# Optimization experiments

Hardware: AMD Instinct MI355X
Metric: run time of the kernel (lower is better)

Reference implementation:

```python
import jax, jax.numpy as jnp
import numpy as np

B, T, D, H = 4, 2048, 1024, 16
HD = D // H

def setup_inputs() -> dict:
    key = jax.random.key(0)
    ks = jax.random.split(key, 7)
    s = 1.0 / np.sqrt(D)
    return {
        "x": jax.random.normal(ks[0], (B, T, D), dtype=jnp.float32),
        "w_qkv": jax.random.uniform(ks[1], (D, 3 * D), jnp.float32, -s, s),
        "b_qkv": jax.random.uniform(ks[2], (3 * D,), jnp.float32, -s, s),
        "w_proj": jax.random.uniform(ks[3], (D, D), jnp.float32, -s, s),
        "b_proj": jax.random.uniform(ks[4], (D,), jnp.float32, -s, s),
        "ln_gamma": jnp.ones((D,), jnp.float32),
        "ln_beta": jnp.zeros((D,), jnp.float32),
    }

def reference(x, w_qkv, b_qkv, w_proj, b_proj, ln_gamma, ln_beta):
    eps = 1e-5
    scale = HD ** -0.5
    residual = x
    # Pre-norm LayerNorm over last dim
    mu = jnp.mean(x, axis=-1, keepdims=True)
    var = jnp.mean(jnp.square(x - mu), axis=-1, keepdims=True)
    xn = (x - mu) * jax.lax.rsqrt(var + eps) * ln_gamma + ln_beta
    # QKV projection: (B,T,3D) -> (3,B,H,T,HD)
    qkv = xn @ w_qkv + b_qkv
    qkv = qkv.reshape(B, T, 3, H, HD).transpose(2, 0, 3, 1, 4)
    q, k, v = qkv[0], qkv[1], qkv[2]
    # Scaled dot-product attention (full T x T scores, as in source)
    attn = jnp.einsum('bhqd,bhkd->bhqk', q, k) * scale
    attn = jax.nn.softmax(attn, axis=-1)
    out = jnp.einsum('bhqk,bhkd->bhqd', attn, v)
    out = out.transpose(0, 2, 1, 3).reshape(B, T, D)
    out = out @ w_proj + b_proj
    return residual + out
```

## Files before the change

kernel.cpp:

```cpp
#include <hip/hip_runtime.h>
#include <cstdint>
#include <cstddef>

#define B_ 4
#define T_ 2048
#define D_ 1024
#define H_ 16

typedef __attribute__((ext_vector_type(8))) short short8;
typedef __attribute__((ext_vector_type(4))) float f32x4;
typedef __attribute__((ext_vector_type(8))) unsigned short u16x8;

__device__ __forceinline__ unsigned short f2b16(float f) {
  union { float f; unsigned int u; } un; un.f = f;
  unsigned int r = un.u + 0x7fffu + ((un.u >> 16) & 1u);
  return (unsigned short)(r >> 16);
}
__device__ __forceinline__ void async_cp16(const void* g, void* l) {
  __builtin_amdgcn_global_load_lds((const __attribute__((address_space(1))) void*)g,
                                   (__attribute__((address_space(3))) void*)l,
                                   16, 0, 0);
}
__device__ __forceinline__ f32x4 mfma16(short8 a, short8 b, f32x4 c) {
  return __builtin_amdgcn_mfma_f32_16x16x32_bf16(a, b, c, 0, 0, 0);
}

__global__ __launch_bounds__(256) void ln_kernel(const float* __restrict__ x,
                                                 const float* __restrict__ gamma,
                                                 const float* __restrict__ beta,
                                                 unsigned short* __restrict__ xn) {
  const int row = blockIdx.x;
  const int t = threadIdx.x;
  const float4 v = ((const float4*)(x + (size_t)row * D_))[t];
  float s  = v.x + v.y + v.z + v.w;
  float s2 = v.x*v.x + v.y*v.y + v.z*v.z + v.w*v.w;
  #pragma unroll
  for (int off = 32; off > 0; off >>= 1) {
    s  += __shfl_down(s, off);
    s2 += __shfl_down(s2, off);
  }
  __shared__ float sh[8];
  const int wv = t >> 6, lane = t & 63;
  if (lane == 0) { sh[wv] = s; sh[4 + wv] = s2; }
  __syncthreads();
  if (t == 0) {
    float ts  = sh[0] + sh[1] + sh[2] + sh[3];
    float ts2 = sh[4] + sh[5] + sh[6] + sh[7];
    float mu  = ts * (1.0f / D_);
    float var = ts2 * (1.0f / D_) - mu * mu;
    sh[0] = mu;
    sh[1] = rsqrtf(var + 1e-5f);
  }
  __syncthreads();
  const float mu = sh[0], rs = sh[1];
  const float4 g  = ((const float4*)gamma)[t];
  const float4 bb = ((const float4*)beta)[t];
  ushort4 o;
  o.x = f2b16((v.x - mu) * rs * g.x + bb.x);
  o.y = f2b16((v.y - mu) * rs * g.y + bb.y);
  o.z = f2b16((v.z - mu) * rs * g.z + bb.z);
  o.w = f2b16((v.w - mu) * rs * g.w + bb.w);
  ((ushort4*)(xn + (size_t)row * D_))[t] = o;
}

__global__ __launch_bounds__(256) void transpose_cast(const float* __restrict__ w,
                                                      unsigned short* __restrict__ wT,
                                                      int K, int N) {
  __shared__ float tile[32][33];
  const int n0 = blockIdx.x * 32;
  const int k0 = blockIdx.y * 32;
  const int tx = threadIdx.x, ty = threadIdx.y;
  #pragma unroll
  for (int i = 0; i < 32; i += 8)
    tile[ty + i][tx] = w[(size_t)(k0 + ty + i) * N + n0 + tx];
  __syncthreads();
  #pragma unroll
  for (int i = 0; i < 32; i += 8)
    wT[(size_t)(n0 + ty + i) * K + k0 + tx] = f2b16(tile[tx][ty + i]);
}

__global__ __launch_bounds__(256) void transpose_v(const unsigned short* __restrict__ vB,
                                                   unsigned short* __restrict__ vtB) {
  __shared__ unsigned short tile[64 * 66];
  const int tid = threadIdx.x;
  const int bh = blockIdx.x;
  const int t0 = blockIdx.y * 64;
  const int lr = tid >> 2, lc = (tid & 3) * 16;
  const unsigned short* src = vB + ((size_t)bh * T_ + t0) * 64;
  *(u16x8*)&tile[lr * 66 + lc]     = *(const u16x8*)(src + (size_t)lr * 64 + lc);
  *(u16x8*)&tile[lr * 66 + lc + 8] = *(const u16x8*)(src + (size_t)lr * 64 + lc + 8);
  __syncthreads();
  const int dv = tid >> 2, cb = (tid & 3) * 16;
  unsigned short outv[16];
  #pragma unroll
  for (int j = 0; j < 16; ++j) {
    const int c = cb + j;
    const int t = (c & 32) | ((c & 4) << 2) | ((c & 16) >> 1) | ((c & 8) >> 1) | (c & 3);
    outv[j] = tile[t * 66 + dv];
  }
  unsigned short* dst = vtB + ((size_t)bh * 64 + dv) * T_ + t0 + cb;
  *(u16x8*)dst       = *(const u16x8*)&outv[0];
  *(u16x8*)(dst + 8) = *(const u16x8*)&outv[8];
}

template <int MODE, int NN>
__global__ __launch_bounds__(512, 2) void gemm8p(const unsigned short* __restrict__ A,
                                                 const unsigned short* __restrict__ Bt,
                                                 const float* __restrict__ bias,
                                                 const float* __restrict__ resid,
                                                 unsigned short* __restrict__ qB,
                                                 unsigned short* __restrict__ kB,
                                                 unsigned short* __restrict__ vB,
                                                 float* __restrict__ outF) {
  constexpr int K = 1024;
  constexpr int NT = 16;
  __shared__ __align__(16) unsigned short As[16384];
  __shared__ __align__(16) unsigned short Bs[32768];

  const int tid  = threadIdx.x;
  const int lane = tid & 63;
  const int wv   = tid >> 6;
  const int l15  = lane & 15, quad = lane >> 4;
  const int wr   = wv >> 1;
  const int wc   = wv & 1;

  constexpr int CPX = (64 * (NN / 256)) / 8;
  const int w = (blockIdx.x & 7) * CPX + (blockIdx.x >> 3);
  const int tileM = (w & 63) * 128;
  const int tileN = (w >> 6) * 256;

  const int sr  = tid >> 3;
  const int scs = ((tid & 7) ^ (sr & 7)) * 8;
  const unsigned short* gA = A  + (size_t)(tileM + sr) * K + scs;
  const unsigned short* gB = Bt + (size_t)(tileN + sr) * K + scs;

  auto stA = [&](int h, int ko, int wb) {
    async_cp16(gA + (size_t)(h * 64) * K + ko, &As[wb * 8192 + h * 4096 + tid * 8]);
  };
  auto stB = [&](int h, int ko, int wb) {
    const unsigned short* g = gB + (size_t)(h * 128) * K + ko;
    unsigned short* l = &Bs[wb * 16384 + h * 8192 + tid * 8];
    async_cp16(g, l);
    async_cp16(g + (size_t)64 * K, l + 4096);
  };

  const int rA  = wr * 16 + l15;
  const int rB  = wc * 64 + l15;
  const int ck0 = ((0 + quad) ^ (l15 & 7)) * 8;
  const int ck1 = ((4 + quad) ^ (l15 & 7)) * 8;

  f32x4 acc[2][2][4] = {};

  stA(0, 0, 0); stB(0, 0, 0); stB(1, 0, 0); stA(1, 0, 0);
  asm volatile("s_waitcnt vmcnt(3)" ::: "memory");
  asm volatile("s_barrier" ::: "memory");

  #pragma unroll 2
  for (int kt = 0; kt < NT; ++kt) {
    const int buf = kt & 1;
    const unsigned short* Ab = &As[buf * 8192];
    const unsigned short* Bb = &Bs[buf * 16384];
    const int wb = buf ^ 1;
    const bool st = (kt + 1) < NT;
    const int ko = (kt + 1) * 64;

    short8 a[2], b0[4][2], b1[4][2];

    a[0] = *(const short8*)&Ab[rA * 64 + ck0];
    a[1] = *(const short8*)&Ab[rA * 64 + ck1];
    #pragma unroll
    for (int fn = 0; fn < 4; ++fn) {
      b0[fn][0] = *(const short8*)&Bb[(rB + fn * 16) * 64 + ck0];
      b0[fn][1] = *(const short8*)&Bb[(rB + fn * 16) * 64 + ck1];
    }
    if (st) stA(0, ko, wb);
    asm volatile("s_waitcnt lgkmcnt(0)" ::: "memory");
    __builtin_amdgcn_sched_barrier(0);
    __builtin_amdgcn_s_setprio(1);
    #pragma unroll
    for (int fn = 0; fn < 4; ++fn) {
      acc[0][0][fn] = mfma16(a[0], b0[fn][0], acc[0][0][fn]);
      acc[0][0][fn] = mfma16(a[1], b0[fn][1], acc[0][0][fn]);
    }
    __builtin_amdgcn_s_setprio(0);
    if (st) asm volatile("s_waitcnt vmcnt(2)" ::: "memory");
    else    asm volatile("s_waitcnt vmcnt(1)" ::: "memory");
    asm volatile("s_barrier" ::: "memory");

    #pragma unroll
    for (int fn = 0; fn < 4; ++fn) {
      b1[fn][0] = *(const short8*)&Bb[8192 + (rB + fn * 16) * 64 + ck0];
      b1[fn][1] = *(const short8*)&Bb[8192 + (rB + fn * 16) * 64 + ck1];
    }
    if (st) stB(0, ko, wb);
    asm volatile("s_waitcnt lgkmcnt(0)" ::: "memory");
    __builtin_amdgcn_sched_barrier(0);
    __builtin_amdgcn_s_setprio(1);
    #pragma unroll
    for (int fn = 0; fn < 4; ++fn) {
      acc[0][1][fn] = mfma16(a[0], b1[fn][0], acc[0][1][fn]);
      acc[0][1][fn] = mfma16(a[1], b1[fn][1], acc[0][1][fn]);
    }
    __builtin_amdgcn_s_setprio(0);
    if (st) asm volatile("s_waitcnt vmcnt(3)" ::: "memory");
    else    asm volatile("s_waitcnt vmcnt(0)" ::: "memory");
    asm volatile("s_barrier" ::: "memory");

    a[0] = *(const short8*)&Ab[4096 + rA * 64 + ck0];
    a[1] = *(const short8*)&Ab[4096 + rA * 64 + ck1];
    if (st) stB(1, ko, wb);
    asm volatile("s_waitcnt lgkmcnt(0)" ::: "memory");
    __builtin_amdgcn_sched_barrier(0);
    __builtin_amdgcn_s_setprio(1);
    #pragma unroll
    for (int fn = 0; fn < 4; ++fn) {
      acc[1][0][fn] = mfma16(a[0], b0[fn][0], acc[1][0][fn]);
      acc[1][0][fn] = mfma16(a[1], b0[fn][1], acc[1][0][fn]);
    }
    __builtin_amdgcn_s_setprio(0);
    asm volatile("s_barrier" ::: "memory");

    if (st) stA(1, ko, wb);
    __builtin_amdgcn_s_setprio(1);
    #pragma unroll
    for (int fn = 0; fn < 4; ++fn) {
      acc[1][1][fn] = mfma16(a[0], b1[fn][0], acc[1][1][fn]);
      acc[1][1][fn] = mfma16(a[1], b1[fn][1], acc[1][1][fn]);
    }
    __builtin_amdgcn_s_setprio(0);
    if (st) asm volatile("s_waitcnt vmcnt(3)" ::: "memory");
    asm volatile("s_barrier" ::: "memory");
  }

  if constexpr (MODE == 0) {
    unsigned short* E = &As[wv * 1152];
    #pragma unroll
    for (int qm = 0; qm < 2; ++qm) {
      #pragma unroll
      for (int qn = 0; qn < 2; ++qn) {
        const int colBase = tileN + qn * 128 + wc * 64;
        const int rowBase = tileM + qm * 64 + wr * 16;
        #pragma unroll
        for (int fn = 0; fn < 4; ++fn) {
          const int col = colBase + fn * 16 + l15;
          const float bv = bias[col];
          const float sc = (col < 1024) ? 0.180336880f : 1.0f;
          #pragma unroll
          for (int r = 0; r < 4; ++r)
            E[(quad * 4 + r) * 72 + fn * 16 + l15] =
                f2b16((acc[qm][qn][fn][r] + bv) * sc);
        }
        const int secq = colBase >> 10;
        const int hh   = (colBase & 1023) >> 6;
        unsigned short* outSec = (secq == 0) ? qB : (secq == 1) ? kB : vB;
        #pragma unroll
        for (int it = 0; it < 2; ++it) {
          const int lrow = it * 8 + (lane >> 3);
          const int row = rowBase + lrow;
          const int b_ = row >> 11, t = row & 2047;
          const u16x8 val = *(const u16x8*)&E[lrow * 72 + (lane & 7) * 8];
          *(u16x8*)(outSec + ((size_t)(b_ * 16 + hh) * T_ + t) * 64 + (lane & 7) * 8) = val;
        }
      }
    }
  } else {
    #pragma unroll
    for (int qm = 0; qm < 2; ++qm) {
      #pragma unroll
      for (int qn = 0; qn < 2; ++qn) {
        #pragma unroll
        for (int fn = 0; fn < 4; ++fn) {
          const int col = tileN + qn * 128 + wc * 64 + fn * 16 + l15;
          const float bv = bias[col];
          #pragma unroll
          for (int r = 0; r < 4; ++r) {
            const int row = tileM + qm * 64 + wr * 16 + quad * 4 + r;
            const size_t idx = (size_t)row * NN + col;
            outF[idx] = acc[qm][qn][fn][r] + bv + resid[idx];
          }
        }
      }
    }
  }
}

__global__ __launch_bounds__(256, 4) void attn_mfma(const unsigned short* __restrict__ qB,
                                                    const unsigned short* __restrict__ kB,
                                                    const unsigned short* __restrict__ vtB,
                                                    unsigned short* __restrict__ aout) {
  __shared__ unsigned short Ks[2][64 * 64];
  __shared__ unsigned short Vs[2][64 * 64];

  const int tid = threadIdx.x;
  const int bid = blockIdx.x;
  const int bh = bid & 63;
  const int qb = bid >> 6;
  const int b = bh >> 4, h = bh & 15;
  const int wv = tid >> 6, lane = tid & 63;
  const int l15 = lane & 15, quad = lane >> 4;

  const unsigned short* qP = qB  + (size_t)bh * T_ * 64;
  const unsigned short* kP = kB  + (size_t)bh * T_ * 64;
  const unsigned short* vP = vtB + (size_t)bh * 64 * T_;
  const int q0 = qb * 128 + wv * 32;

  short8 qf[2][2];
  #pragma unroll
  for (int mi = 0; mi < 2; ++mi)
    #pragma unroll
    for (int ks = 0; ks < 2; ++ks)
      qf[mi][ks] = *(const short8*)(qP + ((size_t)(q0 + mi * 16 + l15)) * 64 + ks * 32 + quad * 8);

  const short8 onesf = {0x3F80, 0x3F80, 0x3F80, 0x3F80, 0x3F80, 0x3F80, 0x3F80, 0x3F80};
  f32x4 accO[2][5] = {};

  const int lrow  = lane >> 3;
  const int lchnk = (lane & 7) ^ (lrow & 7);
  const size_t kOff0 = (size_t)((wv * 2 + 0) * 8 + lrow) * 64 + lchnk * 8;
  const size_t kOff1 = (size_t)((wv * 2 + 1) * 8 + lrow) * 64 + lchnk * 8;
  const size_t vOff0 = (size_t)((wv * 2 + 0) * 8 + lrow) * T_ + lchnk * 8;
  const size_t vOff1 = (size_t)((wv * 2 + 1) * 8 + lrow) * T_ + lchnk * 8;
  const int lOff0 = (wv * 2 + 0) * 512 + lane * 8;
  const int lOff1 = (wv * 2 + 1) * 512 + lane * 8;

  async_cp16(kP + kOff0, &Ks[0][lOff0]);
  async_cp16(kP + kOff1, &Ks[0][lOff1]);
  async_cp16(vP + vOff0, &Vs[0][lOff0]);
  async_cp16(vP + vOff1, &Vs[0][lOff1]);
  __syncthreads();

  for (int kt = 0; kt < 32; ++kt) {
    const int buf = kt & 1;
    if (kt + 1 < 32) {
      const unsigned short* kg = kP + (size_t)(kt + 1) * 64 * 64;
      const unsigned short* vg = vP + (kt + 1) * 64;
      async_cp16(kg + kOff0, &Ks[buf ^ 1][lOff0]);
      async_cp16(kg + kOff1, &Ks[buf ^ 1][lOff1]);
      async_cp16(vg + vOff0, &Vs[buf ^ 1][lOff0]);
      async_cp16(vg + vOff1, &Vs[buf ^ 1][lOff1]);
    }
    const unsigned short* K_ = Ks[buf];
    const unsigned short* V_ = Vs[buf];

    f32x4 accT[4][2] = {};
    #pragma unroll
    for (int ks = 0; ks < 2; ++ks) {
      #pragma unroll
      for (int cc = 0; cc < 4; ++cc) {
        const short8 kb = *(const short8*)&K_[(cc * 16 + l15) * 64 +
                                              (((ks << 2) | quad) ^ (l15 & 7)) * 8];
        accT[cc][0] = mfma16(kb, qf[0][ks], accT[cc][0]);
        accT[cc][1] = mfma16(kb, qf[1][ks], accT[cc][1]);
      }
    }

    short8 pa[2][2];
    #pragma unroll
    for (int mi = 0; mi < 2; ++mi) {
      #pragma unroll
      for (int ks = 0; ks < 2; ++ks) {
        union { unsigned short u[8]; short8 s; } pk;
        #pragma unroll
        for (int r = 0; r < 4; ++r) {
          union { float f; unsigned int u; } e0, e1;
          e0.f = __builtin_amdgcn_exp2f(accT[2 * ks + 0][mi][r]);
          e1.f = __builtin_amdgcn_exp2f(accT[2 * ks + 1][mi][r]);
          pk.u[r]     = (unsigned short)(e0.u >> 16);
          pk.u[4 + r] = (unsigned short)(e1.u >> 16);
        }
        pa[mi][ks] = pk.s;
      }
    }

    #pragma unroll
    for (int ks = 0; ks < 2; ++ks) {
      short8 vb[4];
      #pragma unroll
      for (int nj = 0; nj < 4; ++nj)
        vb[nj] = *(const short8*)&V_[(nj * 16 + l15) * 64 +
                                     (((ks << 2) | quad) ^ (l15 & 7)) * 8];
      #pragma unroll
      for (int mi = 0; mi < 2; ++mi) {
        #pragma unroll
        for (int nj = 0; nj < 4; ++nj)
          accO[mi][nj] = mfma16(pa[mi][ks], vb[nj], accO[mi][nj]);
        accO[mi][4] = mfma16(pa[mi][ks], onesf, accO[mi][4]);
      }
    }

    __syncthreads();
  }

  #pragma unroll
  for (int mi = 0; mi < 2; ++mi) {
    #pragma unroll
    for (int r = 0; r < 4; ++r) {
      const float inv = 1.0f / accO[mi][4][r];
      const int row = q0 + mi * 16 + quad * 4 + r;
      unsigned short* op = aout + (size_t)(b * T_ + row) * D_ + h * 64 + l15;
      #pragma unroll
      for (int nj = 0; nj < 4; ++nj)
        op[nj * 16] = f2b16(accO[mi][nj][r] * inv);
    }
  }
}

extern "C" void kernel_launch(void* const* d_in, const int* in_sizes, int n_in,
                              void* d_out, int out_size, void* d_ws, size_t ws_size,
                              hipStream_t stream) {
  const float* x      = (const float*)d_in[0];
  const float* w_qkv  = (const float*)d_in[1];
  const float* b_qkv  = (const float*)d_in[2];
  const float* w_proj = (const float*)d_in[3];
  const float* b_proj = (const float*)d_in[4];
  const float* ln_g   = (const float*)d_in[5];
  const float* ln_b   = (const float*)d_in[6];
  float* out = (float*)d_out;

  char* ws = (char*)d_ws;
  unsigned short* xn   = (unsigned short*)(ws);
  unsigned short* wTq  = (unsigned short*)(ws + (size_t)(16 << 20));
  unsigned short* wTp  = (unsigned short*)(ws + (size_t)(22 << 20));
  unsigned short* qBuf = (unsigned short*)(ws + (size_t)(24 << 20));
  unsigned short* kBuf = (unsigned short*)(ws + (size_t)(40 << 20));
  unsigned short* vBuf = (unsigned short*)(ws + (size_t)(56 << 20));
  unsigned short* vtB  = (unsigned short*)(ws + (size_t)(72 << 20));
  unsigned short* aout = xn;

  ln_kernel<<<8192, 256, 0, stream>>>(x, ln_g, ln_b, xn);
  transpose_cast<<<dim3(96, 32), dim3(32, 8), 0, stream>>>(w_qkv, wTq, 1024, 3072);
  transpose_cast<<<dim3(32, 32), dim3(32, 8), 0, stream>>>(w_proj, wTp, 1024, 1024);
  gemm8p<0, 3072><<<768, 512, 0, stream>>>(xn, wTq, b_qkv, nullptr,
                                           qBuf, kBuf, vBuf, nullptr);
  transpose_v<<<dim3(64, 32), 256, 0, stream>>>(vBuf, vtB);
  attn_mfma<<<1024, 256, 0, stream>>>(qBuf, kBuf, vtB, aout);
  gemm8p<1, 1024><<<256, 512, 0, stream>>>(aout, wTp, b_proj, x,
                                           nullptr, nullptr, nullptr, out);
}
```

Before: 270.2 us.

## Fuse prep kernels, rewrite GEMM with single-buffer tiles, fuse V transpose into epilogue

Merges LayerNorm and both weight transpose-casts into one prep launch. Replaces the hand-pipelined double-buffered GEMM with a simpler single-buffer GEMM: 256x256 tiles for QKV and 128x128 for the output projection, with more blocks per CU. The QKV epilogue now writes V directly in transposed layout through shared memory, so the separate transpose_v kernel is gone. Priority hints are added around the MFMA sections of the attention kernel. The trade-off is that global-to-LDS loads no longer overlap with compute in the GEMM, which may expose memory latency.

```diff
diff --git a/kernel.cpp b/kernel.cpp
--- a/kernel.cpp
+++ b/kernel.cpp
@@ -25,260 +25,242 @@
   return __builtin_amdgcn_mfma_f32_16x16x32_bf16(a, b, c, 0, 0, 0);
 }
 
-__global__ __launch_bounds__(256) void ln_kernel(const float* __restrict__ x,
-                                                 const float* __restrict__ gamma,
-                                                 const float* __restrict__ beta,
-                                                 unsigned short* __restrict__ xn) {
-  const int row = blockIdx.x;
+__global__ __launch_bounds__(256) void prep_kernel(const float* __restrict__ x,
+                                                   const float* __restrict__ gamma,
+                                                   const float* __restrict__ beta,
+                                                   unsigned short* __restrict__ xn,
+                                                   const float* __restrict__ wq,
+                                                   unsigned short* __restrict__ wTq,
+                                                   const float* __restrict__ wp,
+                                                   unsigned short* __restrict__ wTp) {
+  __shared__ float sh[8];
+  __shared__ float tile[32][33];
+  const int bid = blockIdx.x;
   const int t = threadIdx.x;
-  const float4 v = ((const float4*)(x + (size_t)row * D_))[t];
-  float s  = v.x + v.y + v.z + v.w;
-  float s2 = v.x*v.x + v.y*v.y + v.z*v.z + v.w*v.w;
-  #pragma unroll
-  for (int off = 32; off > 0; off >>= 1) {
-    s  += __shfl_down(s, off);
-    s2 += __shfl_down(s2, off);
+
+  if (bid < 8192) {
+    const int row = bid;
+    const float4 v = ((const float4*)(x + (size_t)row * D_))[t];
+    float s  = v.x + v.y + v.z + v.w;
+    float s2 = v.x*v.x + v.y*v.y + v.z*v.z + v.w*v.w;
+    #pragma unroll
+    for (int off = 32; off > 0; off >>= 1) {
+      s  += __shfl_down(s, off);
+      s2 += __shfl_down(s2, off);
+    }
+    const int wv = t >> 6, lane = t & 63;
+    if (lane == 0) { sh[wv] = s; sh[4 + wv] = s2; }
+    __syncthreads();
+    if (t == 0) {
+      float ts  = sh[0] + sh[1] + sh[2] + sh[3];
+      float ts2 = sh[4] + sh[5] + sh[6] + sh[7];
+      float mu  = ts * (1.0f / D_);
+      float var = ts2 * (1.0f / D_) - mu * mu;
+      sh[0] = mu;
+      sh[1] = rsqrtf(var + 1e-5f);
+    }
+    __syncthreads();
+    const float mu = sh[0], rs = sh[1];
+    const float4 g  = ((const float4*)gamma)[t];
+    const float4 bb = ((const float4*)beta)[t];
+    ushort4 o;
+    o.x = f2b16((v.x - mu) * rs * g.x + bb.x);
+    o.y = f2b16((v.y - mu) * rs * g.y + bb.y);
+    o.z = f2b16((v.z - mu) * rs * g.z + bb.z);
+    o.w = f2b16((v.w - mu) * rs * g.w + bb.w);
+    ((ushort4*)(xn + (size_t)row * D_))[t] = o;
+  } else {
+    const float* w; unsigned short* wT; int K, N, bx, by;
+    if (bid < 8192 + 3072) {
+      const int idx = bid - 8192;
+      w = wq; wT = wTq; K = 1024; N = 3072; bx = idx % 96; by = idx / 96;
+    } else {
+      const int idx = bid - 11264;
+      w = wp; wT = wTp; K = 1024; N = 1024; bx = idx % 32; by = idx / 32;
+    }
+    const int n0 = bx * 32, k0 = by * 32;
+    const int tx = t & 31, ty = t >> 5;
+    #pragma unroll
+    for (int i = 0; i < 32; i += 8)
+      tile[ty + i][tx] = w[(size_t)(k0 + ty + i) * N + n0 + tx];
+    __syncthreads();
+    #pragma unroll
+    for (int i = 0; i < 32; i += 8)
+      wT[(size_t)(n0 + ty + i) * K + k0 + tx] = f2b16(tile[tx][ty + i]);
   }
-  __shared__ float sh[8];
-  const int wv = t >> 6, lane = t & 63;
-  if (lane == 0) { sh[wv] = s; sh[4 + wv] = s2; }
-  __syncthreads();
-  if (t == 0) {
-    float ts  = sh[0] + sh[1] + sh[2] + sh[3];
-    float ts2 = sh[4] + sh[5] + sh[6] + sh[7];
-    float mu  = ts * (1.0f / D_);
-    float var = ts2 * (1.0f / D_) - mu * mu;
-    sh[0] = mu;
-    sh[1] = rsqrtf(var + 1e-5f);
-  }
-  __syncthreads();
-  const float mu = sh[0], rs = sh[1];
-  const float4 g  = ((const float4*)gamma)[t];
-  const float4 bb = ((const float4*)beta)[t];
-  ushort4 o;
-  o.x = f2b16((v.x - mu) * rs * g.x + bb.x);
-  o.y = f2b16((v.y - mu) * rs * g.y + bb.y);
-  o.z = f2b16((v.z - mu) * rs * g.z + bb.z);
-  o.w = f2b16((v.w - mu) * rs * g.w + bb.w);
-  ((ushort4*)(xn + (size_t)row * D_))[t] = o;
-}
-
-__global__ __launch_bounds__(256) void transpose_cast(const float* __restrict__ w,
-                                                      unsigned short* __restrict__ wT,
-                                                      int K, int N) {
-  __shared__ float tile[32][33];
-  const int n0 = blockIdx.x * 32;
-  const int k0 = blockIdx.y * 32;
-  const int tx = threadIdx.x, ty = threadIdx.y;
-  #pragma unroll
-  for (int i = 0; i < 32; i += 8)
-    tile[ty + i][tx] = w[(size_t)(k0 + ty + i) * N + n0 + tx];
-  __syncthreads();
-  #pragma unroll
-  for (int i = 0; i < 32; i += 8)
-    wT[(size_t)(n0 + ty + i) * K + k0 + tx] = f2b16(tile[tx][ty + i]);
-}
-
-__global__ __launch_bounds__(256) void transpose_v(const unsigned short* __restrict__ vB,
-                                                   unsigned short* __restrict__ vtB) {
-  __shared__ unsigned short tile[64 * 66];
-  const int tid = threadIdx.x;
-  const int bh = blockIdx.x;
-  const int t0 = blockIdx.y * 64;
-  const int lr = tid >> 2, lc = (tid & 3) * 16;
-  const unsigned short* src = vB + ((size_t)bh * T_ + t0) * 64;
-  *(u16x8*)&tile[lr * 66 + lc]     = *(const u16x8*)(src + (size_t)lr * 64 + lc);
-  *(u16x8*)&tile[lr * 66 + lc + 8] = *(const u16x8*)(src + (size_t)lr * 64 + lc + 8);
-  __syncthreads();
-  const int dv = tid >> 2, cb = (tid & 3) * 16;
-  unsigned short outv[16];
-  #pragma unroll
-  for (int j = 0; j < 16; ++j) {
-    const int c = cb + j;
-    const int t = (c & 32) | ((c & 4) << 2) | ((c & 16) >> 1) | ((c & 8) >> 1) | (c & 3);
-    outv[j] = tile[t * 66 + dv];
-  }
-  unsigned short* dst = vtB + ((size_t)bh * 64 + dv) * T_ + t0 + cb;
-  *(u16x8*)dst       = *(const u16x8*)&outv[0];
-  *(u16x8*)(dst + 8) = *(const u16x8*)&outv[8];
 }
 
 template <int MODE, int NN>
-__global__ __launch_bounds__(512, 2) void gemm8p(const unsigned short* __restrict__ A,
-                                                 const unsigned short* __restrict__ Bt,
-                                                 const float* __restrict__ bias,
-                                                 const float* __restrict__ resid,
-                                                 unsigned short* __restrict__ qB,
-                                                 unsigned short* __restrict__ kB,
-                                                 unsigned short* __restrict__ vB,
-                                                 float* __restrict__ outF) {
-  constexpr int K = 1024;
+__global__ __launch_bounds__(512, 4) void gemm_sb(const unsigned short* __restrict__ A,
+                                                  const unsigned short* __restrict__ Bt,
+                                                  const float* __restrict__ bias,
+                                                  const float* __restrict__ resid,
+                                                  unsigned short* __restrict__ qB,
+                                                  unsigned short* __restrict__ kB,
+                                                  unsigned short* __restrict__ vtB,
+                                                  float* __restrict__ outF) {
+  constexpr int K  = 1024;
   constexpr int NT = 16;
-  __shared__ __align__(16) unsigned short As[16384];
-  __shared__ __align__(16) unsigned short Bs[32768];
+  constexpr int BM = (MODE == 0) ? 256 : 128;
+  constexpr int FM = (MODE == 0) ? 2 : 1;
+  constexpr int FN = (MODE == 0) ? 4 : 2;
+  constexpr int ASH = BM * 64;
+  __shared__ __align__(16) unsigned short S[2 * ASH];
 
   const int tid  = threadIdx.x;
   const int lane = tid & 63;
   const int wv   = tid >> 6;
   const int l15  = lane & 15, quad = lane >> 4;
-  const int wr   = wv >> 1;
-  const int wc   = wv & 1;
-
-  constexpr int CPX = (64 * (NN / 256)) / 8;
+  const int wr   = wv >> 1, wc = wv & 1;
+
+  constexpr int MT  = 8192 / BM;
+  constexpr int NTL = NN / BM;
+  constexpr int CPX = (MT * NTL) / 8;
   const int w = (blockIdx.x & 7) * CPX + (blockIdx.x >> 3);
-  const int tileM = (w & 63) * 128;
-  const int tileN = (w >> 6) * 256;
+  const int tileM = (w % MT) * BM;
+  const int tileN = (w / MT) * BM;
 
   const int sr  = tid >> 3;
   const int scs = ((tid & 7) ^ (sr & 7)) * 8;
   const unsigned short* gA = A  + (size_t)(tileM + sr) * K + scs;
   const unsigned short* gB = Bt + (size_t)(tileN + sr) * K + scs;
 
-  auto stA = [&](int h, int ko, int wb) {
-    async_cp16(gA + (size_t)(h * 64) * K + ko, &As[wb * 8192 + h * 4096 + tid * 8]);
-  };
-  auto stB = [&](int h, int ko, int wb) {
-    const unsigned short* g = gB + (size_t)(h * 128) * K + ko;
-    unsigned short* l = &Bs[wb * 16384 + h * 8192 + tid * 8];
-    async_cp16(g, l);
-    async_cp16(g + (size_t)64 * K, l + 4096);
-  };
-
-  const int rA  = wr * 16 + l15;
-  const int rB  = wc * 64 + l15;
-  const int ck0 = ((0 + quad) ^ (l15 & 7)) * 8;
-  const int ck1 = ((4 + quad) ^ (l15 & 7)) * 8;
-
-  f32x4 acc[2][2][4] = {};
-
-  stA(0, 0, 0); stB(0, 0, 0); stB(1, 0, 0); stA(1, 0, 0);
-  asm volatile("s_waitcnt vmcnt(3)" ::: "memory");
-  asm volatile("s_barrier" ::: "memory");
-
-  #pragma unroll 2
+  const int rA = wr * (BM / 8) + l15;
+  const int rB = wc * (BM / 4) + l15;
+
+  f32x4 acc[2][2][FM][FN] = {};
+
   for (int kt = 0; kt < NT; ++kt) {
-    const int buf = kt & 1;
-    const unsigned short* Ab = &As[buf * 8192];
-    const unsigned short* Bb = &Bs[buf * 16384];
-    const int wb = buf ^ 1;
-    const bool st = (kt + 1) < NT;
-    const int ko = (kt + 1) * 64;
-
-    short8 a[2], b0[4][2], b1[4][2];
-
-    a[0] = *(const short8*)&Ab[rA * 64 + ck0];
-    a[1] = *(const short8*)&Ab[rA * 64 + ck1];
-    #pragma unroll
-    for (int fn = 0; fn < 4; ++fn) {
-      b0[fn][0] = *(const short8*)&Bb[(rB + fn * 16) * 64 + ck0];
-      b0[fn][1] = *(const short8*)&Bb[(rB + fn * 16) * 64 + ck1];
-    }
-    if (st) stA(0, ko, wb);
-    asm volatile("s_waitcnt lgkmcnt(0)" ::: "memory");
-    __builtin_amdgcn_sched_barrier(0);
-    __builtin_amdgcn_s_setprio(1);
-    #pragma unroll
-    for (int fn = 0; fn < 4; ++fn) {
-      acc[0][0][fn] = mfma16(a[0], b0[fn][0], acc[0][0][fn]);
-      acc[0][0][fn] = mfma16(a[1], b0[fn][1], acc[0][0][fn]);
-    }
-    __builtin_amdgcn_s_setprio(0);
-    if (st) asm volatile("s_waitcnt vmcnt(2)" ::: "memory");
-    else    asm volatile("s_waitcnt vmcnt(1)" ::: "memory");
-    asm volatile("s_barrier" ::: "memory");
-
-    #pragma unroll
-    for (int fn = 0; fn < 4; ++fn) {
-      b1[fn][0] = *(const short8*)&Bb[8192 + (rB + fn * 16) * 64 + ck0];
-      b1[fn][1] = *(const short8*)&Bb[8192 + (rB + fn * 16) * 64 + ck1];
-    }
-    if (st) stB(0, ko, wb);
-    asm volatile("s_waitcnt lgkmcnt(0)" ::: "memory");
-    __builtin_amdgcn_sched_barrier(0);
-    __builtin_amdgcn_s_setprio(1);
-    #pragma unroll
-    for (int fn = 0; fn < 4; ++fn) {
-      acc[0][1][fn] = mfma16(a[0], b1[fn][0], acc[0][1][fn]);
-      acc[0][1][fn] = mfma16(a[1], b1[fn][1], acc[0][1][fn]);
-    }
-    __builtin_amdgcn_s_setprio(0);
-    if (st) asm volatile("s_waitcnt vmcnt(3)" ::: "memory");
-    else    asm volatile("s_waitcnt vmcnt(0)" ::: "memory");
-    asm volatile("s_barrier" ::: "memory");
-
-    a[0] = *(const short8*)&Ab[4096 + rA * 64 + ck0];
-    a[1] = *(const short8*)&Ab[4096 + rA * 64 + ck1];
-    if (st) stB(1, ko, wb);
-    asm volatile("s_waitcnt lgkmcnt(0)" ::: "memory");
-    __builtin_amdgcn_sched_barrier(0);
-    __builtin_amdgcn_s_setprio(1);
-    #pragma unroll
-    for (int fn = 0; fn < 4; ++fn) {
-      acc[1][0][fn] = mfma16(a[0], b0[fn][0], acc[1][0][fn]);
-      acc[1][0][fn] = mfma16(a[1], b0[fn][1], acc[1][0][fn]);
-    }
-    __builtin_amdgcn_s_setprio(0);
-    asm volatile("s_barrier" ::: "memory");
-
-    if (st) stA(1, ko, wb);
-    __builtin_amdgcn_s_setprio(1);
-    #pragma unroll
-    for (int fn = 0; fn < 4; ++fn) {
-      acc[1][1][fn] = mfma16(a[0], b1[fn][0], acc[1][1][fn]);
-      acc[1][1][fn] = mfma16(a[1], b1[fn][1], acc[1][1][fn]);
-    }
-    __builtin_amdgcn_s_setprio(0);
-    if (st) asm volatile("s_waitcnt vmcnt(3)" ::: "memory");
-    asm volatile("s_barrier" ::: "memory");
+    if (kt) __syncthreads();
+    const int ko = kt * 64;
+    #pragma unroll
+    for (int p = 0; p < BM / 64; ++p) {
+      async_cp16(gA + (size_t)(p * 64) * K + ko, &S[p * 4096 + tid * 8]);
+      async_cp16(gB + (size_t)(p * 64) * K + ko, &S[ASH + p * 4096 + tid * 8]);
+    }
+    __syncthreads();
+
+    #pragma unroll
+    for (int ks = 0; ks < 2; ++ks) {
+      const int ck = (((ks << 2) | quad) ^ (l15 & 7)) * 8;
+      short8 a[2 * FM];
+      #pragma unroll
+      for (int qm = 0; qm < 2; ++qm)
+        #pragma unroll
+        for (int fm = 0; fm < FM; ++fm)
+          a[qm * FM + fm] = *(const short8*)&S[qm * (ASH / 2) + (rA + fm * 16) * 64 + ck];
+      #pragma unroll
+      for (int qn = 0; qn < 2; ++qn) {
+        short8 b[FN];
+        #pragma unroll
+        for (int fn = 0; fn < FN; ++fn)
+          b[fn] = *(const short8*)&S[ASH + qn * (ASH / 2) + (rB + fn * 16) * 64 + ck];
+        __builtin_amdgcn_s_setprio(1);
+        #pragma unroll
+        for (int qm = 0; qm < 2; ++qm)
+          #pragma unroll
+          for (int fm = 0; fm < FM; ++fm)
+            #pragma unroll
+            for (int fn = 0; fn < FN; ++fn)
+              acc[qm][qn][fm][fn] = mfma16(a[qm * FM + fm], b[fn], acc[qm][qn][fm][fn]);
+        __builtin_amdgcn_s_setprio(0);
+      }
+    }
   }
-
-  if constexpr (MODE == 0) {
-    unsigned short* E = &As[wv * 1152];
+  __syncthreads();
+
+  if constexpr (MODE == 1) {
+    #pragma unroll
+    for (int qm = 0; qm < 2; ++qm)
+      #pragma unroll
+      for (int qn = 0; qn < 2; ++qn)
+        #pragma unroll
+        for (int fn = 0; fn < FN; ++fn) {
+          const int col = tileN + qn * 64 + wc * 32 + fn * 16 + l15;
+          const float bv = bias[col];
+          #pragma unroll
+          for (int r = 0; r < 4; ++r) {
+            const int row = tileM + qm * 64 + wr * 16 + quad * 4 + r;
+            const size_t idx = (size_t)row * NN + col;
+            outF[idx] = acc[qm][qn][0][fn][r] + bv + resid[idx];
+          }
+        }
+  } else if (tileN < 2048) {
+    unsigned short* E = &S[wv * 2304];
     #pragma unroll
     for (int qm = 0; qm < 2; ++qm) {
       #pragma unroll
       for (int qn = 0; qn < 2; ++qn) {
         const int colBase = tileN + qn * 128 + wc * 64;
-        const int rowBase = tileM + qm * 64 + wr * 16;
+        const int rowBase = tileM + qm * 128 + wr * 32;
         #pragma unroll
         for (int fn = 0; fn < 4; ++fn) {
           const int col = colBase + fn * 16 + l15;
           const float bv = bias[col];
           const float sc = (col < 1024) ? 0.180336880f : 1.0f;
           #pragma unroll
-          for (int r = 0; r < 4; ++r)
-            E[(quad * 4 + r) * 72 + fn * 16 + l15] =
-                f2b16((acc[qm][qn][fn][r] + bv) * sc);
+          for (int fm = 0; fm < 2; ++fm)
+            #pragma unroll
+            for (int r = 0; r < 4; ++r)
+              E[(fm * 16 + quad * 4 + r) * 72 + fn * 16 + l15] =
+                  f2b16((acc[qm][qn][fm][fn][r] + bv) * sc);
         }
         const int secq = colBase >> 10;
         const int hh   = (colBase & 1023) >> 6;
-        unsigned short* outSec = (secq == 0) ? qB : (secq == 1) ? kB : vB;
-        #pragma unroll
-        for (int it = 0; it < 2; ++it) {
+        unsigned short* outSec = (secq == 0) ? qB : kB;
+        #pragma unroll
+        for (int it = 0; it < 4; ++it) {
           const int lrow = it * 8 + (lane >> 3);
           const int row = rowBase + lrow;
-          const int b_ = row >> 11, t = row & 2047;
+          const int b_ = row >> 11, tt = row & 2047;
           const u16x8 val = *(const u16x8*)&E[lrow * 72 + (lane & 7) * 8];
-          *(u16x8*)(outSec + ((size_t)(b_ * 16 + hh) * T_ + t) * 64 + (lane & 7) * 8) = val;
+          *(u16x8*)(outSec + ((size_t)(b_ * 16 + hh) * T_ + tt) * 64 + (lane & 7) * 8) = val;
         }
       }
     }
   } else {
+    const int b_    = tileM >> 11;
+    const int tbase = tileM & 2047;
+    const int h0    = (tileN - 2048) >> 6;
+    const int myTb  = wr >> 1;
+    const int cpr   = 32 * (wr & 1) + 8 * quad;
     #pragma unroll
     for (int qm = 0; qm < 2; ++qm) {
       #pragma unroll
-      for (int qn = 0; qn < 2; ++qn) {
-        #pragma unroll
-        for (int fn = 0; fn < 4; ++fn) {
-          const int col = tileN + qn * 128 + wc * 64 + fn * 16 + l15;
-          const float bv = bias[col];
+      for (int tb = 0; tb < 2; ++tb) {
+        if (myTb == tb) {
           #pragma unroll
-          for (int r = 0; r < 4; ++r) {
-            const int row = tileM + qm * 64 + wr * 16 + quad * 4 + r;
-            const size_t idx = (size_t)row * NN + col;
-            outF[idx] = acc[qm][qn][fn][r] + bv + resid[idx];
+          for (int qn = 0; qn < 2; ++qn) {
+            const int head = qn * 2 + wc;
+            const int colBase = tileN + qn * 128 + wc * 64;
+            #pragma unroll
+            for (int fn = 0; fn < 4; ++fn) {
+              const int dv = fn * 16 + l15;
+              const float bv = bias[colBase + fn * 16 + l15];
+              #pragma unroll
+              for (int fm = 0; fm < 2; ++fm)
+                #pragma unroll
+                for (int r = 0; r < 4; ++r)
+                  S[head * 4608 + dv * 72 + cpr + 4 * fm + r] =
+                      f2b16(acc[qm][qn][fm][fn][r] + bv);
+            }
           }
         }
+        __syncthreads();
+        {
+          const int head = wv & 3;
+          const int dvh  = wv >> 2;
+          const size_t base = ((size_t)(b_ * 16 + h0 + head) * 64) * T_ +
+                              tbase + qm * 128 + tb * 64;
+          const int c4 = (lane & 15) * 4;
+          #pragma unroll
+          for (int i = 0; i < 8; ++i) {
+            const int dv = dvh * 32 + i * 4 + (lane >> 4);
+            const ushort4 val = *(const ushort4*)&S[head * 4608 + dv * 72 + c4];
+            *(ushort4*)(vtB + base + (size_t)dv * T_ + c4) = val;
+          }
+        }
+        __syncthreads();
       }
     }
   }
@@ -343,6 +325,7 @@
     const unsigned short* V_ = Vs[buf];
 
     f32x4 accT[4][2] = {};
+    __builtin_amdgcn_s_setprio(1);
     #pragma unroll
     for (int ks = 0; ks < 2; ++ks) {
       #pragma unroll
@@ -353,6 +336,7 @@
         accT[cc][1] = mfma16(kb, qf[1][ks], accT[cc][1]);
       }
     }
+    __builtin_amdgcn_s_setprio(0);
 
     short8 pa[2][2];
     #pragma unroll
@@ -372,6 +356,7 @@
       }
     }
 
+    __builtin_amdgcn_s_setprio(1);
     #pragma unroll
     for (int ks = 0; ks < 2; ++ks) {
       short8 vb[4];
@@ -387,6 +372,7 @@
         accO[mi][4] = mfma16(pa[mi][ks], onesf, accO[mi][4]);
       }
     }
+    __builtin_amdgcn_s_setprio(0);
 
     __syncthreads();
   }
@@ -423,17 +409,13 @@
   unsigned short* wTp  = (unsigned short*)(ws + (size_t)(22 << 20));
   unsigned short* qBuf = (unsigned short*)(ws + (size_t)(24 << 20));
   unsigned short* kBuf = (unsigned short*)(ws + (size_t)(40 << 20));
-  unsigned short* vBuf = (unsigned short*)(ws + (size_t)(56 << 20));
   unsigned short* vtB  = (unsigned short*)(ws + (size_t)(72 << 20));
   unsigned short* aout = xn;
 
-  ln_kernel<<<8192, 256, 0, stream>>>(x, ln_g, ln_b, xn);
-  transpose_cast<<<dim3(96, 32), dim3(32, 8), 0, stream>>>(w_qkv, wTq, 1024, 3072);
-  transpose_cast<<<dim3(32, 32), dim3(32, 8), 0, stream>>>(w_proj, wTp, 1024, 1024);
-  gemm8p<0, 3072><<<768, 512, 0, stream>>>(xn, wTq, b_qkv, nullptr,
-                                           qBuf, kBuf, vBuf, nullptr);
-  transpose_v<<<dim3(64, 32), 256, 0, stream>>>(vBuf, vtB);
+  prep_kernel<<<12288, 256, 0, stream>>>(x, ln_g, ln_b, xn, w_qkv, wTq, w_proj, wTp);
+  gemm_sb<0, 3072><<<384, 512, 0, stream>>>(xn, wTq, b_qkv, nullptr,
+                                            qBuf, kBuf, vtB, nullptr);
   attn_mfma<<<1024, 256, 0, stream>>>(qBuf, kBuf, vtB, aout);
-  gemm8p<1, 1024><<<256, 512, 0, stream>>>(aout, wTp, b_proj, x,
-                                           nullptr, nullptr, nullptr, out);
-}
+  gemm_sb<1, 1024><<<512, 512, 0, stream>>>(aout, wTp, b_proj, x,
+                                            nullptr, nullptr, nullptr, out);
+}
```

Measured after the change: 683.9 us. 153% more time.
